# Kernel optimization log

Hardware: AMD Instinct MI355X
Metric: run time of the kernel (lower is better)

The kernel has to match this reference:

```python
import jax, jax.numpy as jnp
import numpy as np

B, T, C, H = 2, 2048, 1024, 16
HD = C // H  # head_dim = 64

def setup_inputs() -> dict:
    key = jax.random.key(0)
    ks = jax.random.split(key, 9)
    s = 1.0 / np.sqrt(C)
    return {
        "x": jax.random.normal(ks[0], (B, T, C), dtype=jnp.float32),
        "Wk": jax.random.uniform(ks[1], (C, C), jnp.float32, -s, s),
        "bk": jax.random.uniform(ks[2], (C,), jnp.float32, -s, s),
        "Wq": jax.random.uniform(ks[3], (C, C), jnp.float32, -s, s),
        "bq": jax.random.uniform(ks[4], (C,), jnp.float32, -s, s),
        "Wv": jax.random.uniform(ks[5], (C, C), jnp.float32, -s, s),
        "bv": jax.random.uniform(ks[6], (C,), jnp.float32, -s, s),
        "Wp": jax.random.uniform(ks[7], (C, C), jnp.float32, -s, s),
        "bp": jax.random.uniform(ks[8], (C,), jnp.float32, -s, s),
    }

def reference(x, Wk, bk, Wq, bq, Wv, bv, Wp, bp):
    # Linear projections: [B,T,C] -> [B,H,T,HD]
    def split_heads(t):
        return t.reshape(B, T, H, HD).transpose(0, 2, 1, 3)
    k = split_heads(x @ Wk.T + bk)
    q = split_heads(x @ Wq.T + bq)
    v = split_heads(x @ Wv.T + bv)
    # scaled dot-product with causal mask
    att = jnp.einsum('bhtd,bhsd->bhts', q, k) * (1.0 / np.sqrt(HD))
    causal = jnp.tril(jnp.ones((T, T), dtype=bool))
    att = jnp.where(causal[None, None], att, -jnp.inf)
    att = jax.nn.softmax(att, axis=-1)
    y = jnp.einsum('bhts,bhsd->bhtd', att, v)  # [B,H,T,HD]
    y = y.transpose(0, 2, 1, 3).reshape(B, T, C)
    return y @ Wp.T + bp
```

## Files before the change

### kernel.cpp

```cpp
#include <hip/hip_runtime.h>
#include <stdint.h>

#define Bv  2
#define Tv  2048
#define Cv  1024
#define Hv  16
#define HDv 64
#define LOG2E 1.44269504088896340736f

typedef __bf16 bf16x8 __attribute__((ext_vector_type(8)));
typedef float f32x4 __attribute__((ext_vector_type(4)));
typedef unsigned short us4v __attribute__((ext_vector_type(4)));
typedef unsigned short us8v __attribute__((ext_vector_type(8)));

#define VMCNT(n) asm volatile("s_waitcnt vmcnt(" #n ")" ::: "memory")
#define LGKM0()  asm volatile("s_waitcnt lgkmcnt(0)" ::: "memory")
#define SBAR()   __builtin_amdgcn_s_barrier()
#define SCHED0() __builtin_amdgcn_sched_barrier(0)

static __device__ __forceinline__ unsigned short f2bf(float f) {
    unsigned int u = __builtin_bit_cast(unsigned int, f);
    u += 0x7FFFu + ((u >> 16) & 1u);
    return (unsigned short)(u >> 16);
}

static __device__ __forceinline__ unsigned int cvt_pk_bf16(float lo, float hi) {
    unsigned int w;
    asm("v_cvt_pk_bf16_f32 %0, %1, %2" : "=v"(w) : "v"(lo), "v"(hi));
    return w;
}

static __device__ __forceinline__ void gld_lds16(const void* g, void* l) {
    __builtin_amdgcn_global_load_lds(
        (const __attribute__((address_space(1))) void*)g,
        (__attribute__((address_space(3))) void*)l, 16, 0, 0);
}

static __device__ __forceinline__ f32x4 mfma_bf16(bf16x8 a, bf16x8 b, f32x4 c) {
    return __builtin_amdgcn_mfma_f32_16x16x32_bf16(a, b, c, 0, 0, 0);
}

static __device__ __forceinline__ f32x4 fmax4(f32x4 a, f32x4 b) {
    f32x4 r;
    r[0] = fmaxf(a[0], b[0]); r[1] = fmaxf(a[1], b[1]);
    r[2] = fmaxf(a[2], b[2]); r[3] = fmaxf(a[3], b[3]);
    return r;
}

__global__ __launch_bounds__(256) void cvt_kernel(const float* __restrict__ in,
                                                  unsigned short* __restrict__ out,
                                                  int n) {
    int i = (blockIdx.x * 256 + threadIdx.x) * 4;
    if (i >= n) return;
    float4 v = *(const float4*)(in + i);
    us4v o;
    o[0] = f2bf(v.x); o[1] = f2bf(v.y); o[2] = f2bf(v.z); o[3] = f2bf(v.w);
    *(us4v*)(out + i) = o;
}

__global__ __launch_bounds__(256) void cvt4_kernel(const float* __restrict__ a,
                                                   const float* __restrict__ b,
                                                   const float* __restrict__ c,
                                                   const float* __restrict__ d,
                                                   unsigned short* __restrict__ oa,
                                                   unsigned short* __restrict__ ob,
                                                   unsigned short* __restrict__ oc,
                                                   unsigned short* __restrict__ od) {
    const int sel = blockIdx.x >> 10;
    const float* in = sel == 0 ? a : sel == 1 ? b : sel == 2 ? c : d;
    unsigned short* out = sel == 0 ? oa : sel == 1 ? ob : sel == 2 ? oc : od;
    int i = ((blockIdx.x & 1023) * 256 + threadIdx.x) * 4;
    float4 v = *(const float4*)(in + i);
    us4v o;
    o[0] = f2bf(v.x); o[1] = f2bf(v.y); o[2] = f2bf(v.z); o[3] = f2bf(v.w);
    *(us4v*)(out + i) = o;
}

__global__ __launch_bounds__(256) void gemm_qkv(const unsigned short* __restrict__ X,
                                                const unsigned short* __restrict__ Wqk,
                                                const unsigned short* __restrict__ Wv,
                                                const float* __restrict__ bq,
                                                const float* __restrict__ bk,
                                                const float* __restrict__ bv,
                                                unsigned short* __restrict__ qout,
                                                unsigned short* __restrict__ vtout,
                                                float scale) {
    __shared__ unsigned short As[2][128 * 32];
    __shared__ unsigned short Bs[2][128 * 32];
    const int K = Cv;

    const int tid  = threadIdx.x;
    const int lane = tid & 63;
    const int w    = tid >> 6;
    const int wr   = w >> 1, wc = w & 1;
    const int l16  = lane & 15;
    const int lk8  = (lane >> 4) * 8;
    const int id   = blockIdx.x;

    if (id < 512) {
        const int n0 = (id & 15) * 128;
        const int m0 = (id >> 4) * 128;
        f32x4 acc[4][4] = {};
        const int srow = tid >> 2;
        const int skc  = (tid & 3) * 8;

        auto stageAB = [&](int buf, int k0) {
            gld_lds16(X   + (size_t)(m0 + srow)      * K + k0 + skc, &As[buf][(size_t)tid * 8]);
            gld_lds16(X   + (size_t)(m0 + srow + 64) * K + k0 + skc, &As[buf][(size_t)(tid + 256) * 8]);
            gld_lds16(Wqk + (size_t)(n0 + srow)      * K + k0 + skc, &Bs[buf][(size_t)tid * 8]);
            gld_lds16(Wqk + (size_t)(n0 + srow + 64) * K + k0 + skc, &Bs[buf][(size_t)(tid + 256) * 8]);
        };

        int buf = 0;
        stageAB(0, 0);
        for (int k0 = 0; k0 < K; k0 += 32) {
            if (k0 + 32 < K) { stageAB(buf ^ 1, k0 + 32); VMCNT(4); }
            else             VMCNT(0);
            SBAR(); SCHED0();

            bf16x8 af[4], bf[4];
#pragma unroll
            for (int mf = 0; mf < 4; ++mf)
                af[mf] = *(const bf16x8*)&As[buf][(wr * 64 + mf * 16 + l16) * 32 + lk8];
#pragma unroll
            for (int nf = 0; nf < 4; ++nf)
                bf[nf] = *(const bf16x8*)&Bs[buf][(wc * 64 + nf * 16 + l16) * 32 + lk8];
#pragma unroll
            for (int mf = 0; mf < 4; ++mf)
#pragma unroll
                for (int nf = 0; nf < 4; ++nf)
                    acc[mf][nf] = mfma_bf16(af[mf], bf[nf], acc[mf][nf]);

            LGKM0(); SBAR();
            buf ^= 1;
        }

#pragma unroll
        for (int mf = 0; mf < 4; ++mf)
#pragma unroll
            for (int nf = 0; nf < 4; ++nf)
#pragma unroll
                for (int r = 0; r < 4; ++r) {
                    int m = m0 + wr * 64 + mf * 16 + (lane >> 4) * 4 + r;
                    int n = n0 + wc * 64 + nf * 16 + l16;
                    int sel = n >> 10, ch = n & 1023;
                    float bia = sel ? bk[ch] : bq[ch];
                    float v = (acc[mf][nf][r] + bia) * (sel ? 1.0f : scale);
                    int b = m >> 11, t = m & (Tv - 1);
                    int h = ch >> 6, d = ch & (HDv - 1);
                    qout[(size_t)sel * 4194304 +
                         (((size_t)(b * Hv + h)) * Tv + t) * HDv + d] = f2bf(v);
                }
    } else {
        const int vid = id - 512;
        const int n0 = (vid & 63) * 64;
        const int m0 = (vid >> 6) * 128;
        f32x4 acc[4][2] = {};

        auto stageV = [&](int buf, int k0) {
#pragma unroll
            for (int i = 0; i < 2; ++i) {
                int ch = i * 256 + tid, r = ch >> 2, cc = (ch & 3) * 8;
                gld_lds16(Wv + (size_t)(m0 + r) * K + k0 + cc, &As[buf][(size_t)ch * 8]);
            }
            {
                int r = tid >> 2, cc = (tid & 3) * 8;
                gld_lds16(X + (size_t)(n0 + r) * K + k0 + cc, &Bs[buf][(size_t)tid * 8]);
            }
        };

        int buf = 0;
        stageV(0, 0);
        for (int k0 = 0; k0 < K; k0 += 32) {
            if (k0 + 32 < K) { stageV(buf ^ 1, k0 + 32); VMCNT(3); }
            else             VMCNT(0);
            SBAR(); SCHED0();

            bf16x8 af[4], bf[2];
#pragma unroll
            for (int mf = 0; mf < 4; ++mf)
                af[mf] = *(const bf16x8*)&As[buf][(wr * 64 + mf * 16 + l16) * 32 + lk8];
#pragma unroll
            for (int nf = 0; nf < 2; ++nf)
                bf[nf] = *(const bf16x8*)&Bs[buf][(wc * 32 + nf * 16 + l16) * 32 + lk8];
#pragma unroll
            for (int mf = 0; mf < 4; ++mf)
#pragma unroll
                for (int nf = 0; nf < 2; ++nf)
                    acc[mf][nf] = mfma_bf16(af[mf], bf[nf], acc[mf][nf]);

            LGKM0(); SBAR();
            buf ^= 1;
        }

#pragma unroll
        for (int mf = 0; mf < 4; ++mf)
#pragma unroll
            for (int nf = 0; nf < 2; ++nf)
#pragma unroll
                for (int r = 0; r < 4; ++r) {
                    int m = m0 + wr * 64 + mf * 16 + (lane >> 4) * 4 + r;
                    int n = n0 + wc * 32 + nf * 16 + l16;
                    float v = acc[mf][nf][r] + bv[m];
                    vtout[((size_t)(n >> 11) * 1024 + m) * Tv + (n & (Tv - 1))] = f2bf(v);
                }
    }
}

__global__ __launch_bounds__(256) void gemm_64(const unsigned short* __restrict__ A,
                                               const unsigned short* __restrict__ Bm,
                                               const float* __restrict__ bias0,
                                               float* __restrict__ out,
                                               int N, int K) {
    __shared__ unsigned short As[2][128 * 64];
    __shared__ unsigned short Bs[2][64 * 64];

    const int tid  = threadIdx.x;
    const int lane = tid & 63;
    const int w    = tid >> 6;
    const int wr   = w >> 1, wc = w & 1;
    const int m0   = blockIdx.y * 128;
    const int n0   = blockIdx.x * 64;
    const int l16  = lane & 15;
    const int lk   = (lane >> 4);

    f32x4 acc[4][2] = {};

    auto stageAB = [&](int buf, int k0) {
#pragma unroll
        for (int i = 0; i < 4; ++i) {
            int ch = i * 256 + tid, r = ch >> 3, cs = ch & 7, c = cs ^ (r & 7);
            gld_lds16(A + (size_t)(m0 + r) * K + k0 + c * 8, &As[buf][(size_t)ch * 8]);
        }
#pragma unroll
        for (int i = 0; i < 2; ++i) {
            int ch = i * 256 + tid, r = ch >> 3, cs = ch & 7, c = cs ^ (r & 7);
            gld_lds16(Bm + (size_t)(n0 + r) * K + k0 + c * 8, &Bs[buf][(size_t)ch * 8]);
        }
    };

    int buf = 0;
    stageAB(0, 0);
    for (int k0 = 0; k0 < K; k0 += 64) {
        if (k0 + 64 < K) { stageAB(buf ^ 1, k0 + 64); VMCNT(6); }
        else             VMCNT(0);
        SBAR(); SCHED0();

#pragma unroll
        for (int ks = 0; ks < 2; ++ks) {
            bf16x8 af[4], bf[2];
#pragma unroll
            for (int mf = 0; mf < 4; ++mf) {
                int row = wr * 64 + mf * 16 + l16;
                af[mf] = *(const bf16x8*)&As[buf][(row * 8 + ((ks * 4 + lk) ^ (row & 7))) * 8];
            }
#pragma unroll
            for (int nf = 0; nf < 2; ++nf) {
                int row = wc * 32 + nf * 16 + l16;
                bf[nf] = *(const bf16x8*)&Bs[buf][(row * 8 + ((ks * 4 + lk) ^ (row & 7))) * 8];
            }
#pragma unroll
            for (int mf = 0; mf < 4; ++mf)
#pragma unroll
                for (int nf = 0; nf < 2; ++nf)
                    acc[mf][nf] = mfma_bf16(af[mf], bf[nf], acc[mf][nf]);
        }

        LGKM0(); SBAR();
        buf ^= 1;
    }

#pragma unroll
    for (int mf = 0; mf < 4; ++mf)
#pragma unroll
        for (int nf = 0; nf < 2; ++nf)
#pragma unroll
            for (int r = 0; r < 4; ++r) {
                int m = m0 + wr * 64 + mf * 16 + (lane >> 4) * 4 + r;
                int n = n0 + wc * 32 + nf * 16 + l16;
                out[(size_t)m * N + n] = acc[mf][nf][r] + bias0[n];
            }
}

__global__ __launch_bounds__(256) void attn_kernel(const unsigned short* __restrict__ q,
                                                   const unsigned short* __restrict__ k,
                                                   const unsigned short* __restrict__ vt,
                                                   unsigned short* __restrict__ y) {
    __shared__ __align__(16) unsigned short Ks[2][128 * 64];
    __shared__ __align__(16) unsigned short Vs[2][64 * 128];
    __shared__ __align__(16) unsigned short Pb[4][16 * 128];

    const int tid  = threadIdx.x;
    const int lane = tid & 63;
    const int w    = tid >> 6;
    const int l16  = lane & 15;
    const int lk   = lane >> 4;

    const int lb   = blockIdx.x;
    const int xcd  = lb & 7;
    const int rest = lb >> 3;
    const int bh   = xcd * 4 + (rest >> 4);
    const int p    = rest & 15;

    const int b = bh >> 4, h = bh & (Hv - 1);
    const size_t head_off = (size_t)bh * (Tv * HDv);
    const unsigned short* kpb = k  + head_off;
    const unsigned short* vpb = vt + head_off;
    unsigned short* pb = &Pb[w][0];
    const int key3 = l16 & 7;
    const int key4 = key3 << 1;
    const int kg0  = (lk ^ key3) * 8;
    const int kg1  = ((4 + lk) ^ key3) * 8;

    bf16x8 ones;
    {
        us8v o;
#pragma unroll
        for (int i = 0; i < 8; ++i) o[i] = 0x3F80;
        ones = __builtin_bit_cast(bf16x8, o);
    }

    auto stage = [&](int buf, int kk0) {
#pragma unroll
        for (int i = 0; i < 4; ++i) {
            int ch = (w * 4 + i) * 64 + lane;
            int r  = ch >> 3, cs = ch & 7, c = cs ^ (r & 7);
            gld_lds16(kpb + (size_t)(kk0 + r) * HDv + c * 8, &Ks[buf][ch * 8]);
        }
#pragma unroll
        for (int i = 0; i < 4; ++i) {
            int ch = (w * 4 + i) * 64 + lane;
            int r  = ch >> 4, cs = ch & 15, c = cs ^ ((r & 7) << 1);
            gld_lds16(vpb + (size_t)r * Tv + kk0 + c * 8, &Vs[buf][ch * 8]);
        }
    };

    for (int ph = 0; ph < 2; ++ph) {
        const int tile = ph ? (31 - p) : p;
        const int qr0  = tile * 64 + w * 16;
        const int qg   = qr0 + l16;
        const int nkt  = (tile + 2) >> 1;

        bf16x8 qf0, qf1;
        {
            const unsigned short* qp = q + head_off + (size_t)qg * HDv + lk * 8;
            qf0 = *(const bf16x8*)qp;
            qf1 = *(const bf16x8*)(qp + 32);
        }

        f32x4 acc[4] = {};
        f32x4 lacc = {};
        float m = -1e38f;

        int cur = 0;
        stage(0, 0);

        for (int j = 0; j < nkt; ++j) {
            const int kk0 = j * 128;
            if (j + 1 < nkt) { stage(cur ^ 1, kk0 + 128); VMCNT(8); }
            else             VMCNT(0);
            SBAR(); SCHED0();

            f32x4 s[8];
            __builtin_amdgcn_s_setprio(1);
#pragma unroll
            for (int ct = 0; ct < 8; ++ct) {
                const int rb = (ct * 16 + l16) * 64;
                bf16x8 k0 = *(const bf16x8*)&Ks[cur][rb + kg0];
                bf16x8 k1 = *(const bf16x8*)&Ks[cur][rb + kg1];
                f32x4 z = {};
                z = mfma_bf16(k0, qf0, z);
                z = mfma_bf16(k1, qf1, z);
                s[ct] = z;
            }
            __builtin_amdgcn_s_setprio(0);

            if (kk0 + 127 > qr0) {
#pragma unroll
                for (int ct = 0; ct < 8; ++ct) {
                    const int kb2 = kk0 + ct * 16 + lk * 4;
#pragma unroll
                    for (int r = 0; r < 4; ++r)
                        if (kb2 + r > qg) s[ct][r] = -1e38f;
                }
            }

            f32x4 t0 = fmax4(fmax4(fmax4(s[0], s[1]), fmax4(s[2], s[3])),
                             fmax4(fmax4(s[4], s[5]), fmax4(s[6], s[7])));
            float pm = fmaxf(fmaxf(t0[0], t0[1]), fmaxf(t0[2], t0[3]));
            pm = fmaxf(pm, __shfl_xor(pm, 16));
            pm = fmaxf(pm, __shfl_xor(pm, 32));

            if (__all(pm - m <= 8.0f)) {
#pragma unroll
                for (int ct = 0; ct < 8; ++ct)
#pragma unroll
                    for (int r = 0; r < 4; ++r)
                        s[ct][r] = __builtin_exp2f(s[ct][r] - m);
            } else {
                const float mnew  = fmaxf(m, pm);
                const float alpha = __builtin_exp2f(m - mnew);
#pragma unroll
                for (int ct = 0; ct < 8; ++ct)
#pragma unroll
                    for (int r = 0; r < 4; ++r)
                        s[ct][r] = __builtin_exp2f(s[ct][r] - mnew);
#pragma unroll
                for (int nt = 0; nt < 4; ++nt)
                    acc[nt] *= alpha;
                lacc *= alpha;
                m = mnew;
            }

#pragma unroll
            for (int ct = 0; ct < 8; ++ct) {
                uint2 wv;
                wv.x = cvt_pk_bf16(s[ct][0], s[ct][1]);
                wv.y = cvt_pk_bf16(s[ct][2], s[ct][3]);
                int gp = (((ct * 2 + (lk >> 1)) ^ key4) * 8) + (lk & 1) * 4;
                *(uint2*)&pb[l16 * 128 + gp] = wv;
            }

            __builtin_amdgcn_s_setprio(1);
#pragma unroll
            for (int kh = 0; kh < 4; ++kh) {
                const int vg = ((kh * 4 + lk) ^ key4) * 8;
                bf16x8 pf = *(const bf16x8*)&pb[l16 * 128 + vg];
#pragma unroll
                for (int nt = 0; nt < 4; ++nt) {
                    bf16x8 vfr = *(const bf16x8*)&Vs[cur][(nt * 16 + l16) * 128 + vg];
                    acc[nt] = mfma_bf16(vfr, pf, acc[nt]);
                }
                lacc = mfma_bf16(ones, pf, lacc);
            }
            __builtin_amdgcn_s_setprio(0);

            LGKM0(); SBAR();
            cur ^= 1;
        }

        const float rl = 1.0f / lacc[0];
        const size_t ybase = ((size_t)(b * Tv + qg)) * Cv + h * HDv + lk * 4;
#pragma unroll
        for (int nt = 0; nt < 4; ++nt) {
            uint2 wv;
            wv.x = cvt_pk_bf16(acc[nt][0] * rl, acc[nt][1] * rl);
            wv.y = cvt_pk_bf16(acc[nt][2] * rl, acc[nt][3] * rl);
            *(uint2*)&y[ybase + nt * 16] = wv;
        }
    }
}

extern "C" void kernel_launch(void* const* d_in, const int* in_sizes, int n_in,
                              void* d_out, int out_size, void* d_ws, size_t ws_size,
                              hipStream_t stream) {
    const float* x  = (const float*)d_in[0];
    const float* Wk = (const float*)d_in[1];
    const float* bk = (const float*)d_in[2];
    const float* Wq = (const float*)d_in[3];
    const float* bq = (const float*)d_in[4];
    const float* Wv = (const float*)d_in[5];
    const float* bv = (const float*)d_in[6];
    const float* Wp = (const float*)d_in[7];
    const float* bp = (const float*)d_in[8];

    unsigned short* ws   = (unsigned short*)d_ws;
    unsigned short* xb   = ws;
    unsigned short* wqkb = xb   + 4194304;
    unsigned short* wvb  = wqkb + 2097152;
    unsigned short* wpb  = wvb  + 1048576;
    unsigned short* qb   = wpb  + 1048576;
    unsigned short* kb   = qb   + 4194304;
    unsigned short* vtb  = kb   + 4194304;
    unsigned short* yb   = xb;
    (void)kb;

    cvt_kernel<<<4096, 256, 0, stream>>>(x, xb, 4194304);
    cvt4_kernel<<<4096, 256, 0, stream>>>(Wq, Wk, Wv, Wp,
                                          wqkb, wqkb + 1048576, wvb, wpb);

    gemm_qkv<<<1024, 256, 0, stream>>>(xb, wqkb, wvb, bq, bk, bv, qb, vtb,
                                       0.125f * LOG2E);

    attn_kernel<<<512, 256, 0, stream>>>(qb, kb, vtb, yb);

    dim3 gp(Cv / 64, (Bv * Tv) / 128);
    gemm_64<<<gp, 256, 0, stream>>>(yb, wpb, bp, (float*)d_out, Cv, Cv);
}
```

Baseline: 127.9 us.

## Merge conversion kernels, unify V-projection tiling to 128x128, change LDS swizzle

The two fp32-to-bf16 conversion launches become one kernel covering x and all four weights, removing a launch. The V projection now uses the same 128x128 tile and staging code as the Q/K path, so the QKV GEMM runs 768 blocks instead of 1024 and each V block does twice the work. The attention kernel's V-tile and P-buffer XOR swizzle changes from key<<1 to key, which alters the LDS bank-conflict pattern. Fewer, larger V blocks raise per-block reuse but lower parallelism, and the swizzle change may add or remove LDS conflicts.

```diff
diff --git a/kernel.cpp b/kernel.cpp
--- a/kernel.cpp
+++ b/kernel.cpp
@@ -47,29 +47,25 @@
     return r;
 }
 
-__global__ __launch_bounds__(256) void cvt_kernel(const float* __restrict__ in,
-                                                  unsigned short* __restrict__ out,
-                                                  int n) {
-    int i = (blockIdx.x * 256 + threadIdx.x) * 4;
-    if (i >= n) return;
-    float4 v = *(const float4*)(in + i);
-    us4v o;
-    o[0] = f2bf(v.x); o[1] = f2bf(v.y); o[2] = f2bf(v.z); o[3] = f2bf(v.w);
-    *(us4v*)(out + i) = o;
-}
-
-__global__ __launch_bounds__(256) void cvt4_kernel(const float* __restrict__ a,
-                                                   const float* __restrict__ b,
-                                                   const float* __restrict__ c,
-                                                   const float* __restrict__ d,
-                                                   unsigned short* __restrict__ oa,
-                                                   unsigned short* __restrict__ ob,
-                                                   unsigned short* __restrict__ oc,
-                                                   unsigned short* __restrict__ od) {
-    const int sel = blockIdx.x >> 10;
-    const float* in = sel == 0 ? a : sel == 1 ? b : sel == 2 ? c : d;
-    unsigned short* out = sel == 0 ? oa : sel == 1 ? ob : sel == 2 ? oc : od;
-    int i = ((blockIdx.x & 1023) * 256 + threadIdx.x) * 4;
+__global__ __launch_bounds__(256) void cvt_all(const float* __restrict__ x,
+                                               const float* __restrict__ wq,
+                                               const float* __restrict__ wk,
+                                               const float* __restrict__ wv,
+                                               const float* __restrict__ wp,
+                                               unsigned short* __restrict__ ox,
+                                               unsigned short* __restrict__ oqk,
+                                               unsigned short* __restrict__ ov,
+                                               unsigned short* __restrict__ op) {
+    const int id = blockIdx.x;
+    const float* in;
+    unsigned short* out;
+    int blk;
+    if (id < 4096)      { in = x;  out = ox;            blk = id; }
+    else if (id < 5120) { in = wq; out = oqk;           blk = id - 4096; }
+    else if (id < 6144) { in = wk; out = oqk + 1048576; blk = id - 5120; }
+    else if (id < 7168) { in = wv; out = ov;            blk = id - 6144; }
+    else                { in = wp; out = op;            blk = id - 7168; }
+    int i = (blk * 256 + threadIdx.x) * 4;
     float4 v = *(const float4*)(in + i);
     us4v o;
     o[0] = f2bf(v.x); o[1] = f2bf(v.y); o[2] = f2bf(v.z); o[3] = f2bf(v.w);
@@ -97,44 +93,47 @@
     const int lk8  = (lane >> 4) * 8;
     const int id   = blockIdx.x;
 
+    const unsigned short *Ap, *Bp;
+    int m0, n0;
+    if (id < 512) { Ap = X;  Bp = Wqk; m0 = (id >> 4) * 128;        n0 = (id & 15) * 128; }
+    else          { Ap = Wv; Bp = X;   m0 = ((id - 512) & 7) * 128; n0 = ((id - 512) >> 3) * 128; }
+
+    f32x4 acc[4][4] = {};
+    const int srow = tid >> 2;
+    const int skc  = (tid & 3) * 8;
+
+    auto stageAB = [&](int buf, int k0) {
+        gld_lds16(Ap + (size_t)(m0 + srow)      * K + k0 + skc, &As[buf][(size_t)tid * 8]);
+        gld_lds16(Ap + (size_t)(m0 + srow + 64) * K + k0 + skc, &As[buf][(size_t)(tid + 256) * 8]);
+        gld_lds16(Bp + (size_t)(n0 + srow)      * K + k0 + skc, &Bs[buf][(size_t)tid * 8]);
+        gld_lds16(Bp + (size_t)(n0 + srow + 64) * K + k0 + skc, &Bs[buf][(size_t)(tid + 256) * 8]);
+    };
+
+    int buf = 0;
+    stageAB(0, 0);
+    for (int k0 = 0; k0 < K; k0 += 32) {
+        if (k0 + 32 < K) { stageAB(buf ^ 1, k0 + 32); VMCNT(4); }
+        else             VMCNT(0);
+        SBAR(); SCHED0();
+
+        bf16x8 af[4], bf[4];
+#pragma unroll
+        for (int mf = 0; mf < 4; ++mf)
+            af[mf] = *(const bf16x8*)&As[buf][(wr * 64 + mf * 16 + l16) * 32 + lk8];
+#pragma unroll
+        for (int nf = 0; nf < 4; ++nf)
+            bf[nf] = *(const bf16x8*)&Bs[buf][(wc * 64 + nf * 16 + l16) * 32 + lk8];
+#pragma unroll
+        for (int mf = 0; mf < 4; ++mf)
+#pragma unroll
+            for (int nf = 0; nf < 4; ++nf)
+                acc[mf][nf] = mfma_bf16(af[mf], bf[nf], acc[mf][nf]);
+
+        LGKM0(); SBAR();
+        buf ^= 1;
+    }
+
     if (id < 512) {
-        const int n0 = (id & 15) * 128;
-        const int m0 = (id >> 4) * 128;
-        f32x4 acc[4][4] = {};
-        const int srow = tid >> 2;
-        const int skc  = (tid & 3) * 8;
-
-        auto stageAB = [&](int buf, int k0) {
-            gld_lds16(X   + (size_t)(m0 + srow)      * K + k0 + skc, &As[buf][(size_t)tid * 8]);
-            gld_lds16(X   + (size_t)(m0 + srow + 64) * K + k0 + skc, &As[buf][(size_t)(tid + 256) * 8]);
-            gld_lds16(Wqk + (size_t)(n0 + srow)      * K + k0 + skc, &Bs[buf][(size_t)tid * 8]);
-            gld_lds16(Wqk + (size_t)(n0 + srow + 64) * K + k0 + skc, &Bs[buf][(size_t)(tid + 256) * 8]);
-        };
-
-        int buf = 0;
-        stageAB(0, 0);
-        for (int k0 = 0; k0 < K; k0 += 32) {
-            if (k0 + 32 < K) { stageAB(buf ^ 1, k0 + 32); VMCNT(4); }
-            else             VMCNT(0);
-            SBAR(); SCHED0();
-
-            bf16x8 af[4], bf[4];
-#pragma unroll
-            for (int mf = 0; mf < 4; ++mf)
-                af[mf] = *(const bf16x8*)&As[buf][(wr * 64 + mf * 16 + l16) * 32 + lk8];
-#pragma unroll
-            for (int nf = 0; nf < 4; ++nf)
-                bf[nf] = *(const bf16x8*)&Bs[buf][(wc * 64 + nf * 16 + l16) * 32 + lk8];
-#pragma unroll
-            for (int mf = 0; mf < 4; ++mf)
-#pragma unroll
-                for (int nf = 0; nf < 4; ++nf)
-                    acc[mf][nf] = mfma_bf16(af[mf], bf[nf], acc[mf][nf]);
-
-            LGKM0(); SBAR();
-            buf ^= 1;
-        }
-
 #pragma unroll
         for (int mf = 0; mf < 4; ++mf)
 #pragma unroll
@@ -152,55 +151,14 @@
                          (((size_t)(b * Hv + h)) * Tv + t) * HDv + d] = f2bf(v);
                 }
     } else {
-        const int vid = id - 512;
-        const int n0 = (vid & 63) * 64;
-        const int m0 = (vid >> 6) * 128;
-        f32x4 acc[4][2] = {};
-
-        auto stageV = [&](int buf, int k0) {
-#pragma unroll
-            for (int i = 0; i < 2; ++i) {
-                int ch = i * 256 + tid, r = ch >> 2, cc = (ch & 3) * 8;
-                gld_lds16(Wv + (size_t)(m0 + r) * K + k0 + cc, &As[buf][(size_t)ch * 8]);
-            }
-            {
-                int r = tid >> 2, cc = (tid & 3) * 8;
-                gld_lds16(X + (size_t)(n0 + r) * K + k0 + cc, &Bs[buf][(size_t)tid * 8]);
-            }
-        };
-
-        int buf = 0;
-        stageV(0, 0);
-        for (int k0 = 0; k0 < K; k0 += 32) {
-            if (k0 + 32 < K) { stageV(buf ^ 1, k0 + 32); VMCNT(3); }
-            else             VMCNT(0);
-            SBAR(); SCHED0();
-
-            bf16x8 af[4], bf[2];
-#pragma unroll
-            for (int mf = 0; mf < 4; ++mf)
-                af[mf] = *(const bf16x8*)&As[buf][(wr * 64 + mf * 16 + l16) * 32 + lk8];
-#pragma unroll
-            for (int nf = 0; nf < 2; ++nf)
-                bf[nf] = *(const bf16x8*)&Bs[buf][(wc * 32 + nf * 16 + l16) * 32 + lk8];
-#pragma unroll
-            for (int mf = 0; mf < 4; ++mf)
-#pragma unroll
-                for (int nf = 0; nf < 2; ++nf)
-                    acc[mf][nf] = mfma_bf16(af[mf], bf[nf], acc[mf][nf]);
-
-            LGKM0(); SBAR();
-            buf ^= 1;
-        }
-
 #pragma unroll
         for (int mf = 0; mf < 4; ++mf)
 #pragma unroll
-            for (int nf = 0; nf < 2; ++nf)
+            for (int nf = 0; nf < 4; ++nf)
 #pragma unroll
                 for (int r = 0; r < 4; ++r) {
                     int m = m0 + wr * 64 + mf * 16 + (lane >> 4) * 4 + r;
-                    int n = n0 + wc * 32 + nf * 16 + l16;
+                    int n = n0 + wc * 64 + nf * 16 + l16;
                     float v = acc[mf][nf][r] + bv[m];
                     vtout[((size_t)(n >> 11) * 1024 + m) * Tv + (n & (Tv - 1))] = f2bf(v);
                 }
@@ -308,7 +266,6 @@
     const unsigned short* vpb = vt + head_off;
     unsigned short* pb = &Pb[w][0];
     const int key3 = l16 & 7;
-    const int key4 = key3 << 1;
     const int kg0  = (lk ^ key3) * 8;
     const int kg1  = ((4 + lk) ^ key3) * 8;
 
@@ -330,7 +287,7 @@
 #pragma unroll
         for (int i = 0; i < 4; ++i) {
             int ch = (w * 4 + i) * 64 + lane;
-            int r  = ch >> 4, cs = ch & 15, c = cs ^ ((r & 7) << 1);
+            int r  = ch >> 4, cs = ch & 15, c = cs ^ (r & 7);
             gld_lds16(vpb + (size_t)r * Tv + kk0 + c * 8, &Vs[buf][ch * 8]);
         }
     };
@@ -417,14 +374,14 @@
                 uint2 wv;
                 wv.x = cvt_pk_bf16(s[ct][0], s[ct][1]);
                 wv.y = cvt_pk_bf16(s[ct][2], s[ct][3]);
-                int gp = (((ct * 2 + (lk >> 1)) ^ key4) * 8) + (lk & 1) * 4;
+                int gp = (((ct * 2 + (lk >> 1)) ^ key3) * 8) + (lk & 1) * 4;
                 *(uint2*)&pb[l16 * 128 + gp] = wv;
             }
 
             __builtin_amdgcn_s_setprio(1);
 #pragma unroll
             for (int kh = 0; kh < 4; ++kh) {
-                const int vg = ((kh * 4 + lk) ^ key4) * 8;
+                const int vg = ((kh * 4 + lk) ^ key3) * 8;
                 bf16x8 pf = *(const bf16x8*)&pb[l16 * 128 + vg];
 #pragma unroll
                 for (int nt = 0; nt < 4; ++nt) {
@@ -475,12 +432,10 @@
     unsigned short* yb   = xb;
     (void)kb;
 
-    cvt_kernel<<<4096, 256, 0, stream>>>(x, xb, 4194304);
-    cvt4_kernel<<<4096, 256, 0, stream>>>(Wq, Wk, Wv, Wp,
-                                          wqkb, wqkb + 1048576, wvb, wpb);
-
-    gemm_qkv<<<1024, 256, 0, stream>>>(xb, wqkb, wvb, bq, bk, bv, qb, vtb,
-                                       0.125f * LOG2E);
+    cvt_all<<<8192, 256, 0, stream>>>(x, Wq, Wk, Wv, Wp, xb, wqkb, wvb, wpb);
+
+    gemm_qkv<<<768, 256, 0, stream>>>(xb, wqkb, wvb, bq, bk, bv, qb, vtb,
+                                      0.125f * LOG2E);
 
     attn_kernel<<<512, 256, 0, stream>>>(qb, kb, vtb, yb);
 
```

After: 129.7 us. No clear change (+1.4%).
